# Performance work log

Hardware: AMD Instinct MI355X
Metric: run time of the kernel (lower is better)

## Reference

```python
import jax, jax.numpy as jnp
import numpy as np

N = 50000      # nodes
E = 800000     # edges (avg degree 16)
D_IN = 128     # node_feature_dim
H = 256        # hidden_dim
EPS = 1e-5     # BatchNorm eps


def setup_inputs() -> dict:
    key = jax.random.key(0)
    ks = jax.random.split(key, 32)
    inp = {
        "x": jax.random.normal(ks[0], (N, D_IN), jnp.float32),
        "edge_index": jax.random.randint(ks[1], (2, E), 0, N, jnp.int32),
    }
    dims = [(D_IN, H), (H, H), (H, H)]
    k = 2
    for i, (din, dout) in enumerate(dims):
        s = 1.0 / np.sqrt(din)
        inp[f"Wl{i}"] = jax.random.uniform(ks[k], (din, dout), jnp.float32, -s, s); k += 1
        inp[f"bl{i}"] = jax.random.uniform(ks[k], (dout,), jnp.float32, -s, s); k += 1
        inp[f"Wr{i}"] = jax.random.uniform(ks[k], (din, dout), jnp.float32, -s, s); k += 1
        inp[f"g{i}"] = jnp.ones((dout,), jnp.float32)
        inp[f"b{i}"] = jnp.zeros((dout,), jnp.float32)
        inp[f"rm{i}"] = jax.random.normal(ks[k], (dout,), jnp.float32) * 0.1; k += 1
        inp[f"rv{i}"] = jax.random.uniform(ks[k], (dout,), jnp.float32, 0.5, 1.5); k += 1
    return inp


def _sage(x, src, dst, Wl, bl, Wr):
    # PyG SAGEConv (aggr='mean'): out = lin_l(mean_{j in N(i)} x_j) + lin_r(x_i)
    deg = jax.ops.segment_sum(jnp.ones((src.shape[0],), x.dtype), dst, num_segments=N)
    agg = jax.ops.segment_sum(x[src], dst, num_segments=N)  # [N, d_in]
    mean = agg / jnp.maximum(deg, 1.0)[:, None]
    return mean @ Wl + bl + x @ Wr


def _bn(x, g, b, rm, rv):
    # eval-mode BatchNorm1d with running stats
    return (x - rm) * (g * jax.lax.rsqrt(rv + EPS)) + b


def reference(x, edge_index,
              Wl0, bl0, Wr0, g0, b0, rm0, rv0,
              Wl1, bl1, Wr1, g1, b1, rm1, rv1,
              Wl2, bl2, Wr2, g2, b2, rm2, rv2):
    src, dst = edge_index[0], edge_index[1]
    h = jax.nn.relu(_bn(_sage(x, src, dst, Wl0, bl0, Wr0), g0, b0, rm0, rv0))
    h = jax.nn.relu(_bn(_sage(h, src, dst, Wl1, bl1, Wr1), g1, b1, rm1, rv1))
    h = _bn(_sage(h, src, dst, Wl2, bl2, Wr2), g2, b2, rm2, rv2)
    return h  # [N, H] node embeddings (dropout is identity in eval mode)
```

## Files before the change

kernel.cpp:

```cpp
#include <hip/hip_runtime.h>
#include <hip/hip_bf16.h>

#define NNODES 50000
#define NEDGES 800000
#define HID 256
#define BN_EPS 1e-5f
#define SCAN_B ((NNODES + 255) / 256)

typedef __attribute__((ext_vector_type(8))) short short8v;
typedef __attribute__((ext_vector_type(4))) float f32x4;
typedef __attribute__((ext_vector_type(2))) float f32x2;

__device__ inline void load_lds16(const void* g, void* l) {
    __builtin_amdgcn_global_load_lds(
        (const __attribute__((address_space(1))) unsigned int*)g,
        (__attribute__((address_space(3))) unsigned int*)l, 16, 0, 0);
}

__global__ void k_countrank(const int* __restrict__ ei, int* __restrict__ cnt,
                            int* __restrict__ rank, int nE) {
    int e = blockIdx.x * blockDim.x + threadIdx.x;
    if (e < nE) rank[e] = atomicAdd(&cnt[ei[nE + e]], 1);
}

__global__ void k_bsum(const int* __restrict__ cnt, int* __restrict__ loc,
                       int* __restrict__ bsum, int n) {
    __shared__ int sh[256];
    int tid = threadIdx.x;
    int i = blockIdx.x * 256 + tid;
    int v = (i < n) ? cnt[i] : 0;
    sh[tid] = v;
    __syncthreads();
    for (int off = 1; off < 256; off <<= 1) {
        int t = (tid >= off) ? sh[tid - off] : 0;
        __syncthreads();
        sh[tid] += t;
        __syncthreads();
    }
    if (i < n) loc[i] = sh[tid] - v;
    if (tid == 255) bsum[blockIdx.x] = sh[255];
}

__global__ void k_bscan(int* __restrict__ bsum, int nb) {
    __shared__ int sh[256];
    int tid = threadIdx.x;
    int v = (tid < nb) ? bsum[tid] : 0;
    sh[tid] = v;
    __syncthreads();
    for (int off = 1; off < 256; off <<= 1) {
        int t = (tid >= off) ? sh[tid - off] : 0;
        __syncthreads();
        sh[tid] += t;
        __syncthreads();
    }
    if (tid < nb) bsum[tid] = sh[tid] - v;
}

__global__ void k_addoff(const int* __restrict__ loc, const int* __restrict__ bsum,
                         int* __restrict__ rowptr, int n, int nE) {
    int i = blockIdx.x * 256 + threadIdx.x;
    if (i < n) rowptr[i] = loc[i] + bsum[blockIdx.x];
    if (i == 0) rowptr[n] = nE;
}

__global__ void k_fill2(const int* __restrict__ ei, const int* __restrict__ rowptr,
                        const int* __restrict__ rank, int* __restrict__ col, int nE) {
    int e = blockIdx.x * blockDim.x + threadIdx.x;
    if (e < nE) col[rowptr[ei[nE + e]] + rank[e]] = ei[e];
}

#define PREP_CAST 1600000
#define PREP_TR   327680
__global__ void k_prep(const float* __restrict__ x,
                       __hip_bfloat16* __restrict__ xb, unsigned char* __restrict__ x8,
                       const float* __restrict__ s0, const float* __restrict__ s1,
                       const float* __restrict__ s2, const float* __restrict__ s3,
                       const float* __restrict__ s4, const float* __restrict__ s5,
                       __hip_bfloat16* __restrict__ d0, __hip_bfloat16* __restrict__ d1,
                       __hip_bfloat16* __restrict__ d2, __hip_bfloat16* __restrict__ d3,
                       __hip_bfloat16* __restrict__ d4, __hip_bfloat16* __restrict__ d5,
                       int* __restrict__ cnt) {
    int f = blockIdx.x * blockDim.x + threadIdx.x;
    if (f < PREP_CAST) {
        float4 v = *(const float4*)(x + f * 4);
        union { uint2 u; unsigned short s[4]; } ob;
        ob.s[0] = __bfloat16_as_ushort(__float2bfloat16(v.x));
        ob.s[1] = __bfloat16_as_ushort(__float2bfloat16(v.y));
        ob.s[2] = __bfloat16_as_ushort(__float2bfloat16(v.z));
        ob.s[3] = __bfloat16_as_ushort(__float2bfloat16(v.w));
        *(uint2*)(xb + f * 4) = ob.u;
        int p = __builtin_amdgcn_cvt_pk_fp8_f32(v.x, v.y, 0, false);
        p = __builtin_amdgcn_cvt_pk_fp8_f32(v.z, v.w, p, true);
        *(int*)(x8 + f * 4) = p;
    } else if (f < PREP_CAST + PREP_TR) {
        int r = f - PREP_CAST;
        const float* src; __hip_bfloat16* dst; int K; int i;
        if (r < 65536) {
            K = 128;
            if (r < 32768) { src = s0; dst = d0; i = r; }
            else           { src = s1; dst = d1; i = r - 32768; }
        } else {
            K = 256;
            int q = r - 65536;
            int wsel = q >> 16;
            i = q & 65535;
            src = (wsel == 0) ? s2 : (wsel == 1) ? s3 : (wsel == 2) ? s4 : s5;
            dst = (wsel == 0) ? d2 : (wsel == 1) ? d3 : (wsel == 2) ? d4 : d5;
        }
        int k = i >> 8;
        int nn = i & 255;
        dst[nn * K + k] = __float2bfloat16(src[i]);
    } else {
        int i = f - PREP_CAST - PREP_TR;
        if (i < NNODES) cnt[i] = 0;
    }
}

template <int D, int U>
__global__ void k_meanf8(const unsigned char* __restrict__ x8,
                         const int* __restrict__ rowptr, const int* __restrict__ col,
                         __hip_bfloat16* __restrict__ mean, int n) {
    constexpr int CPL = D / 16;
    constexpr int R = 64 / CPL;
    int gw = (blockIdx.x * blockDim.x + threadIdx.x) >> 6;
    int lane = threadIdx.x & 63;
    if (gw >= n) return;
    int beg = rowptr[gw], end = rowptr[gw + 1];
    int sub = lane / CPL;
    int fpos = lane % CPL;
    const uint4* base = (const uint4*)x8;

    float acc[16];
#pragma unroll
    for (int j = 0; j < 16; j++) acc[j] = 0.f;

    for (int p0 = beg; p0 < end; p0 += U * R) {
        int idx[U]; bool ok[U];
#pragma unroll
        for (int u = 0; u < U; u++) {
            int p = p0 + u * R + sub;
            ok[u] = (p < end);
            idx[u] = ok[u] ? col[p] : 0;
        }
        uint4 v[U];
#pragma unroll
        for (int u = 0; u < U; u++) {
            uint4 t = {0u, 0u, 0u, 0u};
            if (ok[u]) t = base[(size_t)idx[u] * CPL + fpos];
            v[u] = t;
        }
#pragma unroll
        for (int u = 0; u < U; u++) {
            const unsigned int uu[4] = {v[u].x, v[u].y, v[u].z, v[u].w};
#pragma unroll
            for (int q = 0; q < 4; q++) {
                f32x2 lo = __builtin_amdgcn_cvt_pk_f32_fp8(uu[q], false);
                f32x2 hi = __builtin_amdgcn_cvt_pk_f32_fp8(uu[q], true);
                acc[4 * q + 0] += lo.x;
                acc[4 * q + 1] += lo.y;
                acc[4 * q + 2] += hi.x;
                acc[4 * q + 3] += hi.y;
            }
        }
    }

    if constexpr (R >= 8) {
#pragma unroll
        for (int j = 0; j < 16; j++) acc[j] += __shfl_xor(acc[j], 8, 64);
    }
#pragma unroll
    for (int j = 0; j < 16; j++) acc[j] += __shfl_xor(acc[j], 16, 64);
#pragma unroll
    for (int j = 0; j < 16; j++) acc[j] += __shfl_xor(acc[j], 32, 64);

    if (sub == 0) {
        float inv = (end > beg) ? 1.f / (float)(end - beg) : 0.f;
        union { uint4 v[2]; unsigned short s[16]; } o;
#pragma unroll
        for (int j = 0; j < 16; j++)
            o.s[j] = __bfloat16_as_ushort(__float2bfloat16(acc[j] * inv));
        uint4* dst = (uint4*)(mean + (size_t)gw * D + fpos * 16);
        dst[0] = o.v[0];
        dst[1] = o.v[1];
    }
}

template <int KH, typename OutT, int RELU, int W8>
__launch_bounds__(512, 4)
__global__ void k_gemm4(const __hip_bfloat16* __restrict__ A1,
                        const __hip_bfloat16* __restrict__ A2,
                        const __hip_bfloat16* __restrict__ W1t,
                        const __hip_bfloat16* __restrict__ W2t,
                        const float* __restrict__ bl,
                        const float* __restrict__ g,
                        const float* __restrict__ bb,
                        const float* __restrict__ rm,
                        const float* __restrict__ rv,
                        OutT* __restrict__ out, unsigned char* __restrict__ out8,
                        int n) {
    constexpr int NSTEP = KH / 16;
    constexpr int NCH = 16 * KH;
    __shared__ uint4 ldsv[4096];
    char* lds = (char*)ldsv;
    int tid = threadIdx.x;
    int l = (blockIdx.x & 7) * (gridDim.x >> 3) + (blockIdx.x >> 3);
    int rb = l >> 2, ct = l & 3;
    int colbase = ct * 64;

#pragma unroll
    for (int it = 0; it < NCH / 512; it++) {
        int j = tid + it * 512;
        int k8 = j >> 6, c = j & 63;
        int cs = c ^ (k8 & 7);
        const __hip_bfloat16* src =
            (k8 < KH / 8) ? (W1t + (size_t)(colbase + cs) * KH + k8 * 8)
                          : (W2t + (size_t)(colbase + cs) * KH + (k8 - KH / 8) * 8);
        load_lds16(src, lds + (size_t)j * 16);
    }

    int lane = tid & 63, wv = tid >> 6;
    int quad = lane >> 4, ml = lane & 15;
    int row0 = rb * 256 + wv * 32;

    const short8v* p1[2];
    const short8v* p2[2];
#pragma unroll
    for (int i = 0; i < 2; i++) {
        int r = row0 + i * 16 + ml;
        if (r > n - 1) r = n - 1;
        p1[i] = (const short8v*)(A1 + (size_t)r * KH) + quad;
        p2[i] = (const short8v*)(A2 + (size_t)r * KH) + quad;
    }

    f32x4 acc[2][4];
#pragma unroll
    for (int i = 0; i < 2; i++)
#pragma unroll
        for (int t = 0; t < 4; t++) acc[i][t] = {0.f, 0.f, 0.f, 0.f};

    short8v ab[4][2];
#pragma unroll
    for (int s = 0; s < 3; s++) {
        const short8v* const* pp = (s < NSTEP / 2) ? p1 : p2;
        int sh = (s < NSTEP / 2) ? s : s - NSTEP / 2;
#pragma unroll
        for (int i = 0; i < 2; i++) ab[s][i] = pp[i][sh * 4];
    }
    __syncthreads();

#pragma unroll
    for (int s = 0; s < NSTEP; s++) {
        int sn = s + 3;
        if (sn < NSTEP) {
            const short8v* const* pp = (sn < NSTEP / 2) ? p1 : p2;
            int sh = (sn < NSTEP / 2) ? sn : sn - NSTEP / 2;
#pragma unroll
            for (int i = 0; i < 2; i++) ab[sn & 3][i] = pp[i][sh * 4];
        }
        int k8 = s * 4 + quad;
#pragma unroll
        for (int t = 0; t < 4; t++) {
            short8v bfr = *(const short8v*)(
                lds + (size_t)((k8 * 64 + ((t * 16 + ml) ^ (k8 & 7))) * 16));
            acc[0][t] = __builtin_amdgcn_mfma_f32_16x16x32_bf16(
                ab[s & 3][0], bfr, acc[0][t], 0, 0, 0);
            acc[1][t] = __builtin_amdgcn_mfma_f32_16x16x32_bf16(
                ab[s & 3][1], bfr, acc[1][t], 0, 0, 0);
        }
    }

    __syncthreads();
    char* scrb = lds + wv * 8192;
#pragma unroll
    for (int t = 0; t < 4; t++) {
        int c = colbase + t * 16 + ml;
        float sv = g[c] * rsqrtf(rv[c] + BN_EPS);
        float tv = (bl[c] - rm[c]) * sv + bb[c];
#pragma unroll
        for (int i = 0; i < 2; i++)
#pragma unroll
            for (int r = 0; r < 4; r++) {
                float v = acc[i][t][r] * sv + tv;
                if (RELU) v = fmaxf(v, 0.f);
                int row = i * 16 + quad * 4 + r;
                int off = row * 256 + (((t * 16 + ml) * 4) ^ ((row & 7) << 4));
                *(float*)(scrb + off) = v;
            }
    }
    int rl8 = lane >> 3, c8 = (lane & 7) * 8;
#pragma unroll
    for (int p = 0; p < 4; p++) {
        int rowl = p * 8 + rl8;
        int row = row0 + rowl;
        int sw = (rowl & 7) << 4;
        f32x4 v0 = *(const f32x4*)(scrb + rowl * 256 + ((c8 * 4) ^ sw));
        f32x4 v1 = *(const f32x4*)(scrb + rowl * 256 + ((c8 * 4 + 16) ^ sw));
        if (row < n) {
            if constexpr (sizeof(OutT) == 2) {
                union { uint4 u; unsigned short s[8]; } o;
                o.s[0] = __bfloat16_as_ushort(__float2bfloat16(v0.x));
                o.s[1] = __bfloat16_as_ushort(__float2bfloat16(v0.y));
                o.s[2] = __bfloat16_as_ushort(__float2bfloat16(v0.z));
                o.s[3] = __bfloat16_as_ushort(__float2bfloat16(v0.w));
                o.s[4] = __bfloat16_as_ushort(__float2bfloat16(v1.x));
                o.s[5] = __bfloat16_as_ushort(__float2bfloat16(v1.y));
                o.s[6] = __bfloat16_as_ushort(__float2bfloat16(v1.z));
                o.s[7] = __bfloat16_as_ushort(__float2bfloat16(v1.w));
                *(uint4*)(out + (size_t)row * HID + colbase + c8) = o.u;
            } else {
                float* dst = (float*)out + (size_t)row * HID + colbase + c8;
                *(f32x4*)dst = v0;
                *(f32x4*)(dst + 4) = v1;
            }
            if constexpr (W8) {
                int lo = __builtin_amdgcn_cvt_pk_fp8_f32(v0.x, v0.y, 0, false);
                lo = __builtin_amdgcn_cvt_pk_fp8_f32(v0.z, v0.w, lo, true);
                int hi = __builtin_amdgcn_cvt_pk_fp8_f32(v1.x, v1.y, 0, false);
                hi = __builtin_amdgcn_cvt_pk_fp8_f32(v1.z, v1.w, hi, true);
                uint2 u2 = {(unsigned)lo, (unsigned)hi};
                *(uint2*)(out8 + (size_t)row * HID + colbase + c8) = u2;
            }
        }
    }
}

extern "C" void kernel_launch(void* const* d_in, const int* in_sizes, int n_in,
                              void* d_out, int out_size, void* d_ws, size_t ws_size,
                              hipStream_t stream) {
    const float* x = (const float*)d_in[0];
    const int* ei = (const int*)d_in[1];
    const float *Wl[3], *blv[3], *Wr[3], *g[3], *bb[3], *rm[3], *rv[3];
    for (int i = 0; i < 3; i++) {
        int b = 2 + i * 7;
        Wl[i]  = (const float*)d_in[b + 0];
        blv[i] = (const float*)d_in[b + 1];
        Wr[i]  = (const float*)d_in[b + 2];
        g[i]   = (const float*)d_in[b + 3];
        bb[i]  = (const float*)d_in[b + 4];
        rm[i]  = (const float*)d_in[b + 5];
        rv[i]  = (const float*)d_in[b + 6];
    }

    char* ob = (char*)d_out;
    __hip_bfloat16* xb = (__hip_bfloat16*)ob;
    __hip_bfloat16* h0 = (__hip_bfloat16*)(ob + (size_t)NNODES * 128 * 2);

    char* w = (char*)d_ws;
    size_t off = 0;
    auto alloc = [&](size_t bytes) {
        void* p = w + off;
        off += (bytes + 255) & ~(size_t)255;
        return p;
    };
    int* rowptr = (int*)alloc((NNODES + 1) * sizeof(int));
    int* cnt    = (int*)alloc(NNODES * sizeof(int));
    int* loc    = (int*)alloc(NNODES * sizeof(int));
    int* bsum   = (int*)alloc(SCAN_B * sizeof(int));
    int* rank   = (int*)alloc(NEDGES * sizeof(int));
    int* col    = (int*)alloc(NEDGES * sizeof(int));
    __hip_bfloat16* meanb = (__hip_bfloat16*)alloc((size_t)NNODES * HID * 2);
    __hip_bfloat16* h1    = (__hip_bfloat16*)alloc((size_t)NNODES * HID * 2);
    unsigned char* x8   = (unsigned char*)alloc((size_t)NNODES * 128);
    unsigned char* h0f8 = (unsigned char*)alloc((size_t)NNODES * HID);
    unsigned char* h1f8 = (unsigned char*)alloc((size_t)NNODES * HID);
    __hip_bfloat16* Wt[6];
    int Ks[6] = {128, 128, 256, 256, 256, 256};
    for (int i = 0; i < 6; i++) Wt[i] = (__hip_bfloat16*)alloc((size_t)Ks[i] * HID * 2);

    int prepTotal = PREP_CAST + PREP_TR + NNODES;
    k_prep<<<(prepTotal + 255) / 256, 256, 0, stream>>>(
        x, xb, x8, Wl[0], Wr[0], Wl[1], Wr[1], Wl[2], Wr[2],
        Wt[0], Wt[1], Wt[2], Wt[3], Wt[4], Wt[5], cnt);

    k_countrank<<<(NEDGES + 255) / 256, 256, 0, stream>>>(ei, cnt, rank, NEDGES);
    k_bsum<<<SCAN_B, 256, 0, stream>>>(cnt, loc, bsum, NNODES);
    k_bscan<<<1, 256, 0, stream>>>(bsum, SCAN_B);
    k_addoff<<<SCAN_B, 256, 0, stream>>>(loc, bsum, rowptr, NNODES, NEDGES);
    k_fill2<<<(NEDGES + 255) / 256, 256, 0, stream>>>(ei, rowptr, rank, col, NEDGES);

    int meanBlocks = (NNODES * 64 + 255) / 256;
    int gemmBlocks = ((NNODES + 255) / 256) * 4;

    k_meanf8<128, 2><<<meanBlocks, 256, 0, stream>>>(x8, rowptr, col, meanb, NNODES);
    k_gemm4<128, __hip_bfloat16, 1, 1><<<gemmBlocks, 512, 0, stream>>>(meanb, xb, Wt[0], Wt[1],
        blv[0], g[0], bb[0], rm[0], rv[0], h0, h0f8, NNODES);

    k_meanf8<256, 4><<<meanBlocks, 256, 0, stream>>>(h0f8, rowptr, col, meanb, NNODES);
    k_gemm4<256, __hip_bfloat16, 1, 1><<<gemmBlocks, 512, 0, stream>>>(meanb, h0, Wt[2], Wt[3],
        blv[1], g[1], bb[1], rm[1], rv[1], h1, h1f8, NNODES);

    k_meanf8<256, 4><<<meanBlocks, 256, 0, stream>>>(h1f8, rowptr, col, meanb, NNODES);
    k_gemm4<256, float, 0, 0><<<gemmBlocks, 512, 0, stream>>>(meanb, h1, Wt[4], Wt[5],
        blv[2], g[2], bb[2], rm[2], rv[2], (float*)d_out, (unsigned char*)nullptr, NNODES);
}
```

Baseline: 404.4 us.

## Restructure GEMM to full-width 128-row tiles with double-buffered streamed weights

Replaces the 256-row by 64-column GEMM tiling, which preloaded the whole weight slice into LDS, with 1024-thread blocks that cover all 256 output columns for 128 rows. Weights are pre-packed into a k-chunked layout and streamed into LDS one 16-wide k-step at a time with double buffering. Each A row is now read by one block instead of four column tiles. The cost is a barrier per k-step and a larger 64 KB LDS footprint per block, which may reduce occupancy.

```diff
diff --git a/kernel.cpp b/kernel.cpp
--- a/kernel.cpp
+++ b/kernel.cpp
@@ -94,13 +94,11 @@
         *(int*)(x8 + f * 4) = p;
     } else if (f < PREP_CAST + PREP_TR) {
         int r = f - PREP_CAST;
-        const float* src; __hip_bfloat16* dst; int K; int i;
+        const float* src; __hip_bfloat16* dst; int i;
         if (r < 65536) {
-            K = 128;
             if (r < 32768) { src = s0; dst = d0; i = r; }
             else           { src = s1; dst = d1; i = r - 32768; }
         } else {
-            K = 256;
             int q = r - 65536;
             int wsel = q >> 16;
             i = q & 65535;
@@ -109,7 +107,7 @@
         }
         int k = i >> 8;
         int nn = i & 255;
-        dst[nn * K + k] = __float2bfloat16(src[i]);
+        dst[((k >> 3) * 256 + nn) * 8 + (k & 7)] = __float2bfloat16(src[i]);
     } else {
         int i = f - PREP_CAST - PREP_TR;
         if (i < NNODES) cnt[i] = 0;
@@ -186,11 +184,10 @@
 }
 
 template <int KH, typename OutT, int RELU, int W8>
-__launch_bounds__(512, 4)
-__global__ void k_gemm4(const __hip_bfloat16* __restrict__ A1,
+__launch_bounds__(1024, 4)
+__global__ void k_gemm6(const __hip_bfloat16* __restrict__ A1,
                         const __hip_bfloat16* __restrict__ A2,
-                        const __hip_bfloat16* __restrict__ W1t,
-                        const __hip_bfloat16* __restrict__ W2t,
+                        const __hip_bfloat16* __restrict__ Wp,
                         const float* __restrict__ bl,
                         const float* __restrict__ g,
                         const float* __restrict__ bb,
@@ -199,28 +196,13 @@
                         OutT* __restrict__ out, unsigned char* __restrict__ out8,
                         int n) {
     constexpr int NSTEP = KH / 16;
-    constexpr int NCH = 16 * KH;
-    __shared__ uint4 ldsv[4096];
-    char* lds = (char*)ldsv;
+    __shared__ char lds[65536];
     int tid = threadIdx.x;
-    int l = (blockIdx.x & 7) * (gridDim.x >> 3) + (blockIdx.x >> 3);
-    int rb = l >> 2, ct = l & 3;
-    int colbase = ct * 64;
-
-#pragma unroll
-    for (int it = 0; it < NCH / 512; it++) {
-        int j = tid + it * 512;
-        int k8 = j >> 6, c = j & 63;
-        int cs = c ^ (k8 & 7);
-        const __hip_bfloat16* src =
-            (k8 < KH / 8) ? (W1t + (size_t)(colbase + cs) * KH + k8 * 8)
-                          : (W2t + (size_t)(colbase + cs) * KH + (k8 - KH / 8) * 8);
-        load_lds16(src, lds + (size_t)j * 16);
-    }
-
+    int rb = blockIdx.x;
     int lane = tid & 63, wv = tid >> 6;
     int quad = lane >> 4, ml = lane & 15;
-    int row0 = rb * 256 + wv * 32;
+    int wr = wv >> 2, wc = wv & 3;
+    int row0 = rb * 128 + wr * 32;
 
     const short8v* p1[2];
     const short8v* p2[2];
@@ -238,87 +220,96 @@
 #pragma unroll
         for (int t = 0; t < 4; t++) acc[i][t] = {0.f, 0.f, 0.f, 0.f};
 
-    short8v ab[4][2];
-#pragma unroll
-    for (int s = 0; s < 3; s++) {
-        const short8v* const* pp = (s < NSTEP / 2) ? p1 : p2;
-        int sh = (s < NSTEP / 2) ? s : s - NSTEP / 2;
-#pragma unroll
-        for (int i = 0; i < 2; i++) ab[s][i] = pp[i][sh * 4];
-    }
+    short8v ab[2][2];
+    const char* wpb = (const char*)Wp;
+
+    load_lds16(wpb + tid * 16, lds + tid * 16);
+    ab[0][0] = p1[0][0];
+    ab[0][1] = p1[1][0];
     __syncthreads();
 
 #pragma unroll
     for (int s = 0; s < NSTEP; s++) {
-        int sn = s + 3;
-        if (sn < NSTEP) {
+        char* buf  = lds + (s & 1) * 16384;
+        char* nbuf = lds + ((s + 1) & 1) * 16384;
+        if (s + 1 < NSTEP) {
+            load_lds16(wpb + (size_t)(s + 1) * 16384 + tid * 16, nbuf + tid * 16);
+            int sn = s + 1;
             const short8v* const* pp = (sn < NSTEP / 2) ? p1 : p2;
             int sh = (sn < NSTEP / 2) ? sn : sn - NSTEP / 2;
-#pragma unroll
-            for (int i = 0; i < 2; i++) ab[sn & 3][i] = pp[i][sh * 4];
-        }
-        int k8 = s * 4 + quad;
+            ab[sn & 1][0] = pp[0][sh * 4];
+            ab[sn & 1][1] = pp[1][sh * 4];
+        }
+        short8v bfr[4];
+#pragma unroll
+        for (int t = 0; t < 4; t++)
+            bfr[t] = *(const short8v*)(
+                buf + (size_t)((quad * 256) + (wc * 64 + t * 16 + ml)) * 16);
 #pragma unroll
         for (int t = 0; t < 4; t++) {
-            short8v bfr = *(const short8v*)(
-                lds + (size_t)((k8 * 64 + ((t * 16 + ml) ^ (k8 & 7))) * 16));
             acc[0][t] = __builtin_amdgcn_mfma_f32_16x16x32_bf16(
-                ab[s & 3][0], bfr, acc[0][t], 0, 0, 0);
+                ab[s & 1][0], bfr[t], acc[0][t], 0, 0, 0);
             acc[1][t] = __builtin_amdgcn_mfma_f32_16x16x32_bf16(
-                ab[s & 3][1], bfr, acc[1][t], 0, 0, 0);
-        }
-    }
-
-    __syncthreads();
-    char* scrb = lds + wv * 8192;
+                ab[s & 1][1], bfr[t], acc[1][t], 0, 0, 0);
+        }
+        __syncthreads();
+    }
+
+    char* scrb = lds + wv * 4096;
+    float sv[4], tv[4];
 #pragma unroll
     for (int t = 0; t < 4; t++) {
-        int c = colbase + t * 16 + ml;
-        float sv = g[c] * rsqrtf(rv[c] + BN_EPS);
-        float tv = (bl[c] - rm[c]) * sv + bb[c];
-#pragma unroll
-        for (int i = 0; i < 2; i++)
+        int c = wc * 64 + t * 16 + ml;
+        sv[t] = g[c] * rsqrtf(rv[c] + BN_EPS);
+        tv[t] = (bl[c] - rm[c]) * sv[t] + bb[c];
+    }
+    int rl8 = lane >> 3, c8 = (lane & 7) * 8;
+#pragma unroll
+    for (int p = 0; p < 2; p++) {
+#pragma unroll
+        for (int t = 0; t < 4; t++) {
 #pragma unroll
             for (int r = 0; r < 4; r++) {
-                float v = acc[i][t][r] * sv + tv;
+                float v = acc[p][t][r] * sv[t] + tv[t];
                 if (RELU) v = fmaxf(v, 0.f);
-                int row = i * 16 + quad * 4 + r;
-                int off = row * 256 + (((t * 16 + ml) * 4) ^ ((row & 7) << 4));
+                int rowl = quad * 4 + r;
+                int off = rowl * 256 + (((t * 16 + ml) * 4) ^ ((rowl & 7) << 4));
                 *(float*)(scrb + off) = v;
             }
-    }
-    int rl8 = lane >> 3, c8 = (lane & 7) * 8;
-#pragma unroll
-    for (int p = 0; p < 4; p++) {
-        int rowl = p * 8 + rl8;
-        int row = row0 + rowl;
-        int sw = (rowl & 7) << 4;
-        f32x4 v0 = *(const f32x4*)(scrb + rowl * 256 + ((c8 * 4) ^ sw));
-        f32x4 v1 = *(const f32x4*)(scrb + rowl * 256 + ((c8 * 4 + 16) ^ sw));
-        if (row < n) {
-            if constexpr (sizeof(OutT) == 2) {
-                union { uint4 u; unsigned short s[8]; } o;
-                o.s[0] = __bfloat16_as_ushort(__float2bfloat16(v0.x));
-                o.s[1] = __bfloat16_as_ushort(__float2bfloat16(v0.y));
-                o.s[2] = __bfloat16_as_ushort(__float2bfloat16(v0.z));
-                o.s[3] = __bfloat16_as_ushort(__float2bfloat16(v0.w));
-                o.s[4] = __bfloat16_as_ushort(__float2bfloat16(v1.x));
-                o.s[5] = __bfloat16_as_ushort(__float2bfloat16(v1.y));
-                o.s[6] = __bfloat16_as_ushort(__float2bfloat16(v1.z));
-                o.s[7] = __bfloat16_as_ushort(__float2bfloat16(v1.w));
-                *(uint4*)(out + (size_t)row * HID + colbase + c8) = o.u;
-            } else {
-                float* dst = (float*)out + (size_t)row * HID + colbase + c8;
-                *(f32x4*)dst = v0;
-                *(f32x4*)(dst + 4) = v1;
-            }
-            if constexpr (W8) {
-                int lo = __builtin_amdgcn_cvt_pk_fp8_f32(v0.x, v0.y, 0, false);
-                lo = __builtin_amdgcn_cvt_pk_fp8_f32(v0.z, v0.w, lo, true);
-                int hi = __builtin_amdgcn_cvt_pk_fp8_f32(v1.x, v1.y, 0, false);
-                hi = __builtin_amdgcn_cvt_pk_fp8_f32(v1.z, v1.w, hi, true);
-                uint2 u2 = {(unsigned)lo, (unsigned)hi};
-                *(uint2*)(out8 + (size_t)row * HID + colbase + c8) = u2;
+        }
+#pragma unroll
+        for (int q = 0; q < 2; q++) {
+            int rowl = q * 8 + rl8;
+            int row = row0 + p * 16 + rowl;
+            int sw = (rowl & 7) << 4;
+            f32x4 v0 = *(const f32x4*)(scrb + rowl * 256 + ((c8 * 4) ^ sw));
+            f32x4 v1 = *(const f32x4*)(scrb + rowl * 256 + ((c8 * 4 + 16) ^ sw));
+            if (row < n) {
+                int c0 = wc * 64 + c8;
+                if constexpr (sizeof(OutT) == 2) {
+                    union { uint4 u; unsigned short s[8]; } o;
+                    o.s[0] = __bfloat16_as_ushort(__float2bfloat16(v0.x));
+                    o.s[1] = __bfloat16_as_ushort(__float2bfloat16(v0.y));
+                    o.s[2] = __bfloat16_as_ushort(__float2bfloat16(v0.z));
+                    o.s[3] = __bfloat16_as_ushort(__float2bfloat16(v0.w));
+                    o.s[4] = __bfloat16_as_ushort(__float2bfloat16(v1.x));
+                    o.s[5] = __bfloat16_as_ushort(__float2bfloat16(v1.y));
+                    o.s[6] = __bfloat16_as_ushort(__float2bfloat16(v1.z));
+                    o.s[7] = __bfloat16_as_ushort(__float2bfloat16(v1.w));
+                    *(uint4*)(out + (size_t)row * HID + c0) = o.u;
+                } else {
+                    float* dst = (float*)out + (size_t)row * HID + c0;
+                    *(f32x4*)dst = v0;
+                    *(f32x4*)(dst + 4) = v1;
+                }
+                if constexpr (W8) {
+                    int lo = __builtin_amdgcn_cvt_pk_fp8_f32(v0.x, v0.y, 0, false);
+                    lo = __builtin_amdgcn_cvt_pk_fp8_f32(v0.z, v0.w, lo, true);
+                    int hi = __builtin_amdgcn_cvt_pk_fp8_f32(v1.x, v1.y, 0, false);
+                    hi = __builtin_amdgcn_cvt_pk_fp8_f32(v1.z, v1.w, hi, true);
+                    uint2 u2 = {(unsigned)lo, (unsigned)hi};
+                    *(uint2*)(out8 + (size_t)row * HID + c0) = u2;
+                }
             }
         }
     }
@@ -363,14 +354,14 @@
     unsigned char* x8   = (unsigned char*)alloc((size_t)NNODES * 128);
     unsigned char* h0f8 = (unsigned char*)alloc((size_t)NNODES * HID);
     unsigned char* h1f8 = (unsigned char*)alloc((size_t)NNODES * HID);
-    __hip_bfloat16* Wt[6];
-    int Ks[6] = {128, 128, 256, 256, 256, 256};
-    for (int i = 0; i < 6; i++) Wt[i] = (__hip_bfloat16*)alloc((size_t)Ks[i] * HID * 2);
+    __hip_bfloat16* Wp0 = (__hip_bfloat16*)alloc((size_t)2 * 128 * 256 * 2);
+    __hip_bfloat16* Wp1 = (__hip_bfloat16*)alloc((size_t)2 * 256 * 256 * 2);
+    __hip_bfloat16* Wp2 = (__hip_bfloat16*)alloc((size_t)2 * 256 * 256 * 2);
 
     int prepTotal = PREP_CAST + PREP_TR + NNODES;
     k_prep<<<(prepTotal + 255) / 256, 256, 0, stream>>>(
         x, xb, x8, Wl[0], Wr[0], Wl[1], Wr[1], Wl[2], Wr[2],
-        Wt[0], Wt[1], Wt[2], Wt[3], Wt[4], Wt[5], cnt);
+        Wp0, Wp0 + 32768, Wp1, Wp1 + 65536, Wp2, Wp2 + 65536, cnt);
 
     k_countrank<<<(NEDGES + 255) / 256, 256, 0, stream>>>(ei, cnt, rank, NEDGES);
     k_bsum<<<SCAN_B, 256, 0, stream>>>(cnt, loc, bsum, NNODES);
@@ -379,17 +370,17 @@
     k_fill2<<<(NEDGES + 255) / 256, 256, 0, stream>>>(ei, rowptr, rank, col, NEDGES);
 
     int meanBlocks = (NNODES * 64 + 255) / 256;
-    int gemmBlocks = ((NNODES + 255) / 256) * 4;
+    int gemmBlocks = (NNODES + 127) / 128;
 
     k_meanf8<128, 2><<<meanBlocks, 256, 0, stream>>>(x8, rowptr, col, meanb, NNODES);
-    k_gemm4<128, __hip_bfloat16, 1, 1><<<gemmBlocks, 512, 0, stream>>>(meanb, xb, Wt[0], Wt[1],
+    k_gemm6<128, __hip_bfloat16, 1, 1><<<gemmBlocks, 1024, 0, stream>>>(meanb, xb, Wp0,
         blv[0], g[0], bb[0], rm[0], rv[0], h0, h0f8, NNODES);
 
     k_meanf8<256, 4><<<meanBlocks, 256, 0, stream>>>(h0f8, rowptr, col, meanb, NNODES);
-    k_gemm4<256, __hip_bfloat16, 1, 1><<<gemmBlocks, 512, 0, stream>>>(meanb, h0, Wt[2], Wt[3],
+    k_gemm6<256, __hip_bfloat16, 1, 1><<<gemmBlocks, 1024, 0, stream>>>(meanb, h0, Wp1,
         blv[1], g[1], bb[1], rm[1], rv[1], h1, h1f8, NNODES);
 
     k_meanf8<256, 4><<<meanBlocks, 256, 0, stream>>>(h1f8, rowptr, col, meanb, NNODES);
-    k_gemm4<256, float, 0, 0><<<gemmBlocks, 512, 0, stream>>>(meanb, h1, Wt[4], Wt[5],
+    k_gemm6<256, float, 0, 0><<<gemmBlocks, 1024, 0, stream>>>(meanb, h1, Wp2,
         blv[2], g[2], bb[2], rm[2], rv[2], (float*)d_out, (unsigned char*)nullptr, NNODES);
 }
```

After: 413.1 us. +2.1%, slower.
